# Optimization experiments

Hardware: AMD Instinct MI355X
Metric: run time of the kernel (lower is better)

The kernel has to match this reference:

```python
import jax, jax.numpy as jnp
import numpy as np

N_NODES = 100000
N_EDGES = 1600000
NODE_F = 8   # augmented node features
EDGE_F = 2   # augmented edge features
GLOB_F = 1
HID = 16
L = 3        # message passing steps

EDGE_IN = GLOB_F + EDGE_F + 2 * NODE_F   # 19
NODE_IN = GLOB_F + EDGE_F + NODE_F       # 11
GLOB_IN = EDGE_F + NODE_F + GLOB_F       # 11


def setup_inputs() -> dict:
    key = jax.random.key(0)
    ks = jax.random.split(key, 20)
    inp = {
        "x": jax.random.normal(ks[0], (N_NODES, NODE_F), dtype=jnp.float32),
        "edge_index": jax.random.randint(ks[1], (2, N_EDGES), 0, N_NODES, dtype=jnp.int32),
        "edge_attr": jax.random.normal(ks[2], (N_EDGES, EDGE_F), dtype=jnp.float32),
        "g": jax.random.normal(ks[3], (1, GLOB_F), dtype=jnp.float32),
    }
    s = 0.1
    inp["edge_W1"] = jax.random.normal(ks[4], (L, EDGE_IN, HID), dtype=jnp.float32) * s
    inp["edge_b1"] = jnp.zeros((L, HID), dtype=jnp.float32)
    inp["edge_W2"] = jax.random.normal(ks[5], (L, HID, EDGE_F), dtype=jnp.float32) * s
    inp["edge_b2"] = jnp.zeros((L, EDGE_F), dtype=jnp.float32)
    inp["node_W1"] = jax.random.normal(ks[6], (L, NODE_IN, HID), dtype=jnp.float32) * s
    inp["node_b1"] = jnp.zeros((L, HID), dtype=jnp.float32)
    inp["node_W2"] = jax.random.normal(ks[7], (L, HID, NODE_F), dtype=jnp.float32) * s
    inp["node_b2"] = jnp.zeros((L, NODE_F), dtype=jnp.float32)
    inp["glob_W1"] = jax.random.normal(ks[8], (L, GLOB_IN, HID), dtype=jnp.float32) * s
    inp["glob_b1"] = jnp.zeros((L, HID), dtype=jnp.float32)
    inp["glob_W2"] = jax.random.normal(ks[9], (L, HID, GLOB_F), dtype=jnp.float32) * s
    inp["glob_b2"] = jnp.zeros((L, GLOB_F), dtype=jnp.float32)
    return inp


def _mlp(h, W1, b1, W2, b2):
    # two-layer MLP with ReLU after first layer only (activate_final=False, no layer_norm)
    return jnp.maximum(h @ W1 + b1, 0.0) @ W2 + b2


def reference(x, edge_index, edge_attr, g,
              edge_W1, edge_b1, edge_W2, edge_b2,
              node_W1, node_b1, node_W2, node_b2,
              glob_W1, glob_b1, glob_W2, glob_b2):
    row, col = edge_index[0], edge_index[1]
    n = x.shape[0]
    for l in range(L):
        g_e = jnp.broadcast_to(g, (row.shape[0], GLOB_F))
        # edge block: gather node features along edges, concat, MLP -> [E, EDGE_F]
        e_in = jnp.concatenate([g_e, x[row], x[col], edge_attr], axis=1)
        edge_emb = _mlp(e_in, edge_W1[l], edge_b1[l], edge_W2[l], edge_b2[l])
        # sum-aggregate edge embeddings to source nodes
        agg = jax.ops.segment_sum(edge_emb, row, num_segments=n)
        g_n = jnp.broadcast_to(g, (n, GLOB_F))
        node_emb = _mlp(jnp.concatenate([g_n, x, agg], axis=1),
                        node_W1[l], node_b1[l], node_W2[l], node_b2[l])
        # global block on mean-aggregated edge/node embeddings
        edge_gl = jnp.mean(edge_emb, axis=0, keepdims=True)
        node_gl = jnp.mean(node_emb, axis=0, keepdims=True)
        g = _mlp(jnp.concatenate([node_gl, edge_gl, g], axis=1),
                 glob_W1[l], glob_b1[l], glob_W2[l], glob_b2[l])
        x, edge_attr = node_emb, edge_emb
    return x  # final node embeddings [N, NODE_F]
```

## Files before the change

### kernel.cpp

```cpp
#include <hip/hip_runtime.h>

#define NN 100000
#define NE 1600000
#define CH 4096
#define NCHUNK ((NE + CH - 1) / CH)
#define NBUCK ((NN + 255) / 256)

__device__ __forceinline__ float wave_red(float v) {
#pragma unroll
    for (int off = 32; off > 0; off >>= 1) v += __shfl_down(v, off, 64);
    return v;
}

__global__ __launch_bounds__(256) void hist_kernel(
    const int* __restrict__ ei, int* __restrict__ hist)
{
    __shared__ int h[NBUCK];
    int t = threadIdx.x, c = blockIdx.x;
    for (int b = t; b < NBUCK; b += 256) h[b] = 0;
    __syncthreads();
    int base = c * CH;
    for (int i = t; i < CH; i += 256) {
        int e = base + i;
        if (e < NE) atomicAdd(&h[ei[e] >> 8], 1);
    }
    __syncthreads();
    for (int b = t; b < NBUCK; b += 256) hist[c * NBUCK + b] = h[b];
}

__global__ __launch_bounds__(512) void bscan_kernel(
    const int* __restrict__ hist, int* __restrict__ baseT, int* __restrict__ colTotal)
{
    __shared__ int buf[2][512];
    int b = blockIdx.x, t = threadIdx.x;
    int v = (t < NCHUNK) ? hist[t * NBUCK + b] : 0;
    buf[0][t] = v;
    __syncthreads();
    int src = 0;
    for (int d = 1; d < 512; d <<= 1) {
        int nv = buf[src][t] + ((t >= d) ? buf[src][t - d] : 0);
        buf[src ^ 1][t] = nv;
        src ^= 1;
        __syncthreads();
    }
    if (t < NCHUNK) baseT[b * NCHUNK + t] = buf[src][t] - v;
    if (t == NCHUNK - 1) colTotal[b] = buf[src][t];
}

__global__ __launch_bounds__(512) void boff_kernel(
    const int* __restrict__ colTotal, int* __restrict__ b_off)
{
    __shared__ int buf[2][512];
    int t = threadIdx.x;
    int v = (t < NBUCK) ? colTotal[t] : 0;
    buf[0][t] = v;
    __syncthreads();
    int src = 0;
    for (int d = 1; d < 512; d <<= 1) {
        int nv = buf[src][t] + ((t >= d) ? buf[src][t - d] : 0);
        buf[src ^ 1][t] = nv;
        src ^= 1;
        __syncthreads();
    }
    if (t < NBUCK) b_off[t] = buf[src][t] - v;
    if (t == NBUCK - 1) b_off[NBUCK] = buf[src][t];
}

__global__ __launch_bounds__(256) void fillb_kernel(
    const int* __restrict__ ei, const float* __restrict__ eattr,
    const int* __restrict__ baseT, const int* __restrict__ b_off,
    float4* __restrict__ rec)
{
    __shared__ int sslot[NBUCK];
    int t = threadIdx.x, c = blockIdx.x;
    for (int b = t; b < NBUCK; b += 256)
        sslot[b] = b_off[b] + baseT[b * NCHUNK + c];
    __syncthreads();
    int base = c * CH;
    for (int i = t; i < CH; i += 256) {
        int e = base + i;
        if (e < NE) {
            int row = ei[e];
            int slot = atomicAdd(&sslot[row >> 8], 1);
            float2 ea = reinterpret_cast<const float2*>(eattr)[e];
            float4 v;
            v.x = __int_as_float(row);
            v.y = __int_as_float(ei[NE + e]);
            v.z = ea.x; v.w = ea.y;
            rec[slot] = v;
        }
    }
}

template <bool WRITE_REC, bool NEED_SUM>
__global__ __launch_bounds__(1024, 4) void fused_kernel(
    float4* __restrict__ rec, const int* __restrict__ b_off,
    const float* __restrict__ gptr,
    const float* __restrict__ eW1, const float* __restrict__ eB1,
    const float* __restrict__ eW2, const float* __restrict__ eB2,
    const float* __restrict__ xin,
    const float* __restrict__ nW1, const float* __restrict__ nB1,
    const float* __restrict__ nW2, const float* __restrict__ nB2,
    float* __restrict__ xout, float* __restrict__ sums)
{
    __shared__ float sPrT[16 * 256];
    __shared__ float sagg[256][2];
    __shared__ float redE[16][2];
    __shared__ float redN[4][8];
    int tid = threadIdx.x;
    if (tid < 512) ((float*)sagg)[tid] = 0.f;

    int n0 = blockIdx.x * 256;
    bool own = (tid < 256) && (n0 + tid < NN);
    if (own) {
        const float4* xi = reinterpret_cast<const float4*>(xin + (size_t)(n0 + tid) * 8);
        float4 a0 = xi[0], a1 = xi[1];
        float xv[8] = {a0.x, a0.y, a0.z, a0.w, a1.x, a1.y, a1.z, a1.w};
        float pr[16];
#pragma unroll
        for (int q = 0; q < 16; q++) pr[q] = 0.f;
#pragma unroll
        for (int k = 0; k < 8; k++) {
            float v = xv[k];
#pragma unroll
            for (int q = 0; q < 16; q++) pr[q] += v * eW1[(1 + k) * 16 + q];
        }
#pragma unroll
        for (int q = 0; q < 16; q++) sPrT[q * 256 + tid] = pr[q];
    }
    __syncthreads();

    int e0 = b_off[blockIdx.x], e1 = b_off[blockIdx.x + 1];

    float gval = gptr[0];
    float gterm[16];
#pragma unroll
    for (int q = 0; q < 16; q++) gterm[q] = eB1[q] + gval * eW1[q];

    float t0 = 0.f, t1 = 0.f;
    for (int e = e0 + tid; e < e1; e += 1024) {
        float4 r = rec[e];
        int row = __float_as_int(r.x);
        int col = __float_as_int(r.y);
        float ea0 = r.z, ea1 = r.w;
        int li = row - n0;
        const float4* xc4 = reinterpret_cast<const float4*>(xin + (size_t)col * 8);
        float4 c0 = xc4[0], c1 = xc4[1];
        float xc[8] = {c0.x, c0.y, c0.z, c0.w, c1.x, c1.y, c1.z, c1.w};
        float h[16];
#pragma unroll
        for (int q = 0; q < 16; q++) h[q] = gterm[q] + sPrT[q * 256 + li];
#pragma unroll
        for (int k = 0; k < 8; k++) {
            float v = xc[k];
#pragma unroll
            for (int q = 0; q < 16; q++) h[q] += v * eW1[(9 + k) * 16 + q];
        }
#pragma unroll
        for (int q = 0; q < 16; q++) {
            h[q] += ea0 * eW1[17 * 16 + q];
            h[q] += ea1 * eW1[18 * 16 + q];
        }
        float s0 = eB2[0], s1 = eB2[1];
#pragma unroll
        for (int q = 0; q < 16; q++) {
            float rr = fmaxf(h[q], 0.f);
            s0 += rr * eW2[2 * q];
            s1 += rr * eW2[2 * q + 1];
        }
        if (WRITE_REC) {
            float4 w;
            w.x = r.x; w.y = r.y; w.z = s0; w.w = s1;
            rec[e] = w;
        }
        atomicAdd(&sagg[li][0], s0);
        atomicAdd(&sagg[li][1], s1);
        t0 += s0; t1 += s1;
    }

    if (NEED_SUM) {
        float r0 = wave_red(t0);
        float r1 = wave_red(t1);
        int wave = tid >> 6, lane = tid & 63;
        if (lane == 0) { redE[wave][0] = r0; redE[wave][1] = r1; }
    }
    __syncthreads();
    if (NEED_SUM && tid == 0) {
        float s0 = 0.f, s1 = 0.f;
#pragma unroll
        for (int w = 0; w < 16; w++) { s0 += redE[w][0]; s1 += redE[w][1]; }
        atomicAdd(&sums[0], s0);
        atomicAdd(&sums[1], s1);
    }

    float out[8];
#pragma unroll
    for (int m = 0; m < 8; m++) out[m] = 0.f;

    if (own) {
        int n = n0 + tid;
        float in[11];
        in[0] = gval;
        const float4* xi = reinterpret_cast<const float4*>(xin + (size_t)n * 8);
        float4 a0 = xi[0], a1 = xi[1];
        in[1] = a0.x; in[2] = a0.y; in[3] = a0.z; in[4] = a0.w;
        in[5] = a1.x; in[6] = a1.y; in[7] = a1.z; in[8] = a1.w;
        in[9] = sagg[tid][0]; in[10] = sagg[tid][1];

        float h[16];
#pragma unroll
        for (int q = 0; q < 16; q++) h[q] = nB1[q];
#pragma unroll
        for (int k = 0; k < 11; k++) {
            float v = in[k];
#pragma unroll
            for (int q = 0; q < 16; q++) h[q] += v * nW1[k * 16 + q];
        }
#pragma unroll
        for (int m = 0; m < 8; m++) out[m] = nB2[m];
#pragma unroll
        for (int q = 0; q < 16; q++) {
            float hq = fmaxf(h[q], 0.f);
#pragma unroll
            for (int m = 0; m < 8; m++) out[m] += hq * nW2[q * 8 + m];
        }
        float4* xo = reinterpret_cast<float4*>(xout + (size_t)n * 8);
        xo[0] = make_float4(out[0], out[1], out[2], out[3]);
        xo[1] = make_float4(out[4], out[5], out[6], out[7]);
    }
    if (NEED_SUM) {
        float r[8];
#pragma unroll
        for (int m = 0; m < 8; m++) r[m] = wave_red(out[m]);
        int wave = tid >> 6, lane = tid & 63;
        if (wave < 4 && lane == 0) {
#pragma unroll
            for (int m = 0; m < 8; m++) redN[wave][m] = r[m];
        }
        __syncthreads();
        if (tid == 0) {
#pragma unroll
            for (int m = 0; m < 8; m++) {
                float s = redN[0][m] + redN[1][m] + redN[2][m] + redN[3][m];
                atomicAdd(&sums[2 + m], s);
            }
        }
    }
}

__global__ void glob_kernel(const float* __restrict__ sums,
                            const float* __restrict__ gold,
                            const float* __restrict__ W1, const float* __restrict__ B1,
                            const float* __restrict__ W2, const float* __restrict__ B2,
                            float* __restrict__ gnew)
{
    if (threadIdx.x == 0 && blockIdx.x == 0) {
        float in[11];
#pragma unroll
        for (int j = 0; j < 8; j++) in[j] = sums[2 + j] * (1.0f / NN);
        in[8] = sums[0] * (1.0f / NE);
        in[9] = sums[1] * (1.0f / NE);
        in[10] = gold[0];
        float acc = B2[0];
#pragma unroll
        for (int j = 0; j < 16; j++) {
            float h = B1[j];
#pragma unroll
            for (int k = 0; k < 11; k++) h += in[k] * W1[k * 16 + j];
            acc += fmaxf(h, 0.f) * W2[j];
        }
        gnew[0] = acc;
    }
}

extern "C" void kernel_launch(void* const* d_in, const int* in_sizes, int n_in,
                              void* d_out, int out_size, void* d_ws, size_t ws_size,
                              hipStream_t stream) {
    const float* x     = (const float*)d_in[0];
    const int*   ei    = (const int*)d_in[1];
    const float* eattr = (const float*)d_in[2];
    const float* g     = (const float*)d_in[3];
    const float* eW1 = (const float*)d_in[4];
    const float* eB1 = (const float*)d_in[5];
    const float* eW2 = (const float*)d_in[6];
    const float* eB2 = (const float*)d_in[7];
    const float* nW1 = (const float*)d_in[8];
    const float* nB1 = (const float*)d_in[9];
    const float* nW2 = (const float*)d_in[10];
    const float* nB2 = (const float*)d_in[11];
    const float* gW1 = (const float*)d_in[12];
    const float* gB1 = (const float*)d_in[13];
    const float* gW2 = (const float*)d_in[14];
    const float* gB2 = (const float*)d_in[15];
    float* out = (float*)d_out;

    char* ws = (char*)d_ws;
    float*  xb0   = (float*)(ws);
    float*  xb1   = (float*)(ws + 3200000);
    int*    b_off = (int*)  (ws + 6400000);
    float*  sums  = (float*)(ws + 6401600);
    float*  g1    = (float*)(ws + 6401728);
    float*  g2    = g1 + 1;
    float4* rec   = (float4*)(ws + 6401792);
    int*    hist     = (int*)xb1;
    int*    baseT    = (int*)((char*)xb1 + 611584);
    int*    colTotal = (int*)((char*)xb1 + 1223168);

    dim3 blk(256);
    dim3 fblk(1024);
    dim3 cgrid(NCHUNK);
    dim3 bgrid(NBUCK);

    hipMemsetAsync(sums, 0, 128, stream);
    hist_kernel<<<cgrid, blk, 0, stream>>>(ei, hist);
    bscan_kernel<<<bgrid, 512, 0, stream>>>(hist, baseT, colTotal);
    boff_kernel<<<1, 512, 0, stream>>>(colTotal, b_off);
    fillb_kernel<<<cgrid, blk, 0, stream>>>(ei, eattr, baseT, b_off, rec);

    fused_kernel<true, true><<<bgrid, fblk, 0, stream>>>(
        rec, b_off, g,
        eW1, eB1, eW2, eB2,
        x, nW1, nB1, nW2, nB2,
        xb0, sums);
    glob_kernel<<<1, 64, 0, stream>>>(sums, g, gW1, gB1, gW2, gB2, g1);

    fused_kernel<true, true><<<bgrid, fblk, 0, stream>>>(
        rec, b_off, g1,
        eW1 + 304, eB1 + 16, eW2 + 32, eB2 + 2,
        xb0, nW1 + 176, nB1 + 16, nW2 + 128, nB2 + 8,
        xb1, sums + 16);
    glob_kernel<<<1, 64, 0, stream>>>(sums + 16, g1, gW1 + 176, gB1 + 16, gW2 + 16, gB2 + 1, g2);

    fused_kernel<false, false><<<bgrid, fblk, 0, stream>>>(
        rec, b_off, g2,
        eW1 + 608, eB1 + 32, eW2 + 64, eB2 + 4,
        xb1, nW1 + 352, nB1 + 32, nW2 + 256, nB2 + 16,
        out, sums);
}
```

Measured before the change: 331.7 us.

## Split edge records into packed keys and attrs, double-buffer them into LDS

Replaces the 16-byte per-edge record with a 4-byte packed key (local row plus column) and a separate float2 attribute/embedding array, which cuts per-edge read and write traffic. Edge chunks are staged into LDS with asynchronous global_load_lds and double-buffered so the next chunk loads while the current one computes. Block size drops from 1024 to 512, and the projected source-node features are stored row-major so each edge reads them as float4. The changes add per-chunk barriers. Layer 2 reads and writes eembS in place, which relies on each edge index being read and written by the same thread.

```diff
diff --git a/kernel.cpp b/kernel.cpp
--- a/kernel.cpp
+++ b/kernel.cpp
@@ -5,11 +5,19 @@
 #define CH 4096
 #define NCHUNK ((NE + CH - 1) / CH)
 #define NBUCK ((NN + 255) / 256)
+#define ECHUNK 1024
 
 __device__ __forceinline__ float wave_red(float v) {
 #pragma unroll
     for (int off = 32; off > 0; off >>= 1) v += __shfl_down(v, off, 64);
     return v;
+}
+
+__device__ __forceinline__ void stage16(void* lds, const void* gsrc) {
+    __builtin_amdgcn_global_load_lds(
+        (const __attribute__((address_space(1))) unsigned int*)gsrc,
+        (__attribute__((address_space(3))) unsigned int*)lds,
+        16, 0, 0);
 }
 
 __global__ __launch_bounds__(256) void hist_kernel(
@@ -69,7 +77,7 @@
 __global__ __launch_bounds__(256) void fillb_kernel(
     const int* __restrict__ ei, const float* __restrict__ eattr,
     const int* __restrict__ baseT, const int* __restrict__ b_off,
-    float4* __restrict__ rec)
+    int* __restrict__ keys, float2* __restrict__ attrS)
 {
     __shared__ int sslot[NBUCK];
     int t = threadIdx.x, c = blockIdx.x;
@@ -82,19 +90,17 @@
         if (e < NE) {
             int row = ei[e];
             int slot = atomicAdd(&sslot[row >> 8], 1);
-            float2 ea = reinterpret_cast<const float2*>(eattr)[e];
-            float4 v;
-            v.x = __int_as_float(row);
-            v.y = __int_as_float(ei[NE + e]);
-            v.z = ea.x; v.w = ea.y;
-            rec[slot] = v;
-        }
-    }
-}
-
-template <bool WRITE_REC, bool NEED_SUM>
-__global__ __launch_bounds__(1024, 4) void fused_kernel(
-    float4* __restrict__ rec, const int* __restrict__ b_off,
+            keys[slot] = ((row & 255) << 17) | ei[NE + e];
+            attrS[slot] = reinterpret_cast<const float2*>(eattr)[e];
+        }
+    }
+}
+
+template <bool WRITE_EMB, bool NEED_SUM>
+__global__ __launch_bounds__(512, 4) void fused_kernel(
+    const int* __restrict__ keys,
+    const float2* __restrict__ ein, float2* __restrict__ eout,
+    const int* __restrict__ b_off,
     const float* __restrict__ gptr,
     const float* __restrict__ eW1, const float* __restrict__ eB1,
     const float* __restrict__ eW2, const float* __restrict__ eB2,
@@ -103,19 +109,24 @@
     const float* __restrict__ nW2, const float* __restrict__ nB2,
     float* __restrict__ xout, float* __restrict__ sums)
 {
-    __shared__ float sPrT[16 * 256];
-    __shared__ float sagg[256][2];
-    __shared__ float redE[16][2];
-    __shared__ float redN[4][8];
+    __shared__ float  sPr[256][20];
+    __shared__ float  sagg[256][2];
+    __shared__ int    kbuf[2][ECHUNK];
+    __shared__ float2 abuf[2][ECHUNK];
+    __shared__ float  redE[8][2];
+    __shared__ float  redN[4][8];
     int tid = threadIdx.x;
-    if (tid < 512) ((float*)sagg)[tid] = 0.f;
+    ((float*)sagg)[tid] = 0.f;
 
     int n0 = blockIdx.x * 256;
+    float gval = gptr[0];
     bool own = (tid < 256) && (n0 + tid < NN);
+    float xv[8];
     if (own) {
         const float4* xi = reinterpret_cast<const float4*>(xin + (size_t)(n0 + tid) * 8);
         float4 a0 = xi[0], a1 = xi[1];
-        float xv[8] = {a0.x, a0.y, a0.z, a0.w, a1.x, a1.y, a1.z, a1.w};
+        xv[0] = a0.x; xv[1] = a0.y; xv[2] = a0.z; xv[3] = a0.w;
+        xv[4] = a1.x; xv[5] = a1.y; xv[6] = a1.z; xv[7] = a1.w;
         float pr[16];
 #pragma unroll
         for (int q = 0; q < 16; q++) pr[q] = 0.f;
@@ -125,62 +136,82 @@
 #pragma unroll
             for (int q = 0; q < 16; q++) pr[q] += v * eW1[(1 + k) * 16 + q];
         }
-#pragma unroll
-        for (int q = 0; q < 16; q++) sPrT[q * 256 + tid] = pr[q];
-    }
-    __syncthreads();
+        float4* pw = reinterpret_cast<float4*>(&sPr[tid][0]);
+#pragma unroll
+        for (int t4 = 0; t4 < 4; t4++)
+            pw[t4] = make_float4(pr[4*t4], pr[4*t4+1], pr[4*t4+2], pr[4*t4+3]);
+    }
 
     int e0 = b_off[blockIdx.x], e1 = b_off[blockIdx.x + 1];
-
-    float gval = gptr[0];
+    int a0 = e0 & ~3;
+    int nc = (e1 - a0 + ECHUNK - 1) / ECHUNK;
+
+    if (tid < 256) stage16(&kbuf[0][tid * 4], keys + a0 + tid * 4);
+    stage16(&abuf[0][tid * 2], ein + a0 + tid * 2);
+
     float gterm[16];
 #pragma unroll
     for (int q = 0; q < 16; q++) gterm[q] = eB1[q] + gval * eW1[q];
 
     float t0 = 0.f, t1 = 0.f;
-    for (int e = e0 + tid; e < e1; e += 1024) {
-        float4 r = rec[e];
-        int row = __float_as_int(r.x);
-        int col = __float_as_int(r.y);
-        float ea0 = r.z, ea1 = r.w;
-        int li = row - n0;
-        const float4* xc4 = reinterpret_cast<const float4*>(xin + (size_t)col * 8);
-        float4 c0 = xc4[0], c1 = xc4[1];
-        float xc[8] = {c0.x, c0.y, c0.z, c0.w, c1.x, c1.y, c1.z, c1.w};
-        float h[16];
-#pragma unroll
-        for (int q = 0; q < 16; q++) h[q] = gterm[q] + sPrT[q * 256 + li];
-#pragma unroll
-        for (int k = 0; k < 8; k++) {
-            float v = xc[k];
-#pragma unroll
-            for (int q = 0; q < 16; q++) h[q] += v * eW1[(9 + k) * 16 + q];
-        }
-#pragma unroll
-        for (int q = 0; q < 16; q++) {
-            h[q] += ea0 * eW1[17 * 16 + q];
-            h[q] += ea1 * eW1[18 * 16 + q];
-        }
-        float s0 = eB2[0], s1 = eB2[1];
-#pragma unroll
-        for (int q = 0; q < 16; q++) {
-            float rr = fmaxf(h[q], 0.f);
-            s0 += rr * eW2[2 * q];
-            s1 += rr * eW2[2 * q + 1];
-        }
-        if (WRITE_REC) {
-            float4 w;
-            w.x = r.x; w.y = r.y; w.z = s0; w.w = s1;
-            rec[e] = w;
-        }
-        atomicAdd(&sagg[li][0], s0);
-        atomicAdd(&sagg[li][1], s1);
-        t0 += s0; t1 += s1;
+    for (int c = 0; c < nc; c++) {
+        __syncthreads();
+        int cur = c & 1;
+        if (c + 1 < nc) {
+            int wb = a0 + (c + 1) * ECHUNK;
+            if (tid < 256) stage16(&kbuf[cur ^ 1][tid * 4], keys + wb + tid * 4);
+            stage16(&abuf[cur ^ 1][tid * 2], ein + wb + tid * 2);
+        }
+        int cbase = a0 + c * ECHUNK;
+#pragma unroll
+        for (int j = 0; j < 2; j++) {
+            int idx = tid + j * 512;
+            int e = cbase + idx;
+            if (e < e0 || e >= e1) continue;
+            int k = kbuf[cur][idx];
+            float2 ea = abuf[cur][idx];
+            int li = k >> 17, col = k & 0x1FFFF;
+            const float4* xc4 = reinterpret_cast<const float4*>(xin + (size_t)col * 8);
+            float4 c0 = xc4[0], c1 = xc4[1];
+            const float4* pr4 = reinterpret_cast<const float4*>(&sPr[li][0]);
+            float4 p0 = pr4[0], p1 = pr4[1], p2 = pr4[2], p3 = pr4[3];
+            float h[16];
+            h[0]  = gterm[0]  + p0.x; h[1]  = gterm[1]  + p0.y;
+            h[2]  = gterm[2]  + p0.z; h[3]  = gterm[3]  + p0.w;
+            h[4]  = gterm[4]  + p1.x; h[5]  = gterm[5]  + p1.y;
+            h[6]  = gterm[6]  + p1.z; h[7]  = gterm[7]  + p1.w;
+            h[8]  = gterm[8]  + p2.x; h[9]  = gterm[9]  + p2.y;
+            h[10] = gterm[10] + p2.z; h[11] = gterm[11] + p2.w;
+            h[12] = gterm[12] + p3.x; h[13] = gterm[13] + p3.y;
+            h[14] = gterm[14] + p3.z; h[15] = gterm[15] + p3.w;
+            float xc[8] = {c0.x, c0.y, c0.z, c0.w, c1.x, c1.y, c1.z, c1.w};
+#pragma unroll
+            for (int kk = 0; kk < 8; kk++) {
+                float v = xc[kk];
+#pragma unroll
+                for (int q = 0; q < 16; q++) h[q] += v * eW1[(9 + kk) * 16 + q];
+            }
+#pragma unroll
+            for (int q = 0; q < 16; q++) {
+                h[q] += ea.x * eW1[17 * 16 + q];
+                h[q] += ea.y * eW1[18 * 16 + q];
+            }
+            float s0 = eB2[0], s1 = eB2[1];
+#pragma unroll
+            for (int q = 0; q < 16; q++) {
+                float rr = fmaxf(h[q], 0.f);
+                s0 += rr * eW2[2 * q];
+                s1 += rr * eW2[2 * q + 1];
+            }
+            if (WRITE_EMB) eout[e] = make_float2(s0, s1);
+            atomicAdd(&sagg[li][0], s0);
+            atomicAdd(&sagg[li][1], s1);
+            t0 += s0; t1 += s1;
+        }
     }
 
     if (NEED_SUM) {
-        float r0 = wave_red(t0);
-        float r1 = wave_red(t1);
+        float r0 = wave_red(t0), r1 = wave_red(t1);
         int wave = tid >> 6, lane = tid & 63;
         if (lane == 0) { redE[wave][0] = r0; redE[wave][1] = r1; }
     }
@@ -188,7 +219,7 @@
     if (NEED_SUM && tid == 0) {
         float s0 = 0.f, s1 = 0.f;
 #pragma unroll
-        for (int w = 0; w < 16; w++) { s0 += redE[w][0]; s1 += redE[w][1]; }
+        for (int w = 0; w < 8; w++) { s0 += redE[w][0]; s1 += redE[w][1]; }
         atomicAdd(&sums[0], s0);
         atomicAdd(&sums[1], s1);
     }
@@ -201,10 +232,8 @@
         int n = n0 + tid;
         float in[11];
         in[0] = gval;
-        const float4* xi = reinterpret_cast<const float4*>(xin + (size_t)n * 8);
-        float4 a0 = xi[0], a1 = xi[1];
-        in[1] = a0.x; in[2] = a0.y; in[3] = a0.z; in[4] = a0.w;
-        in[5] = a1.x; in[6] = a1.y; in[7] = a1.z; in[8] = a1.w;
+#pragma unroll
+        for (int k = 0; k < 8; k++) in[1 + k] = xv[k];
         in[9] = sagg[tid][0]; in[10] = sagg[tid][1];
 
         float h[16];
@@ -301,13 +330,15 @@
     float*  sums  = (float*)(ws + 6401600);
     float*  g1    = (float*)(ws + 6401728);
     float*  g2    = g1 + 1;
-    float4* rec   = (float4*)(ws + 6401792);
+    int*    keys  = (int*)  (ws + 6401792);
+    float2* attrS = (float2*)(ws + 12809984);
+    float2* eembS = (float2*)(ws + 25626368);
     int*    hist     = (int*)xb1;
     int*    baseT    = (int*)((char*)xb1 + 611584);
     int*    colTotal = (int*)((char*)xb1 + 1223168);
 
     dim3 blk(256);
-    dim3 fblk(1024);
+    dim3 fblk(512);
     dim3 cgrid(NCHUNK);
     dim3 bgrid(NBUCK);
 
@@ -315,24 +346,24 @@
     hist_kernel<<<cgrid, blk, 0, stream>>>(ei, hist);
     bscan_kernel<<<bgrid, 512, 0, stream>>>(hist, baseT, colTotal);
     boff_kernel<<<1, 512, 0, stream>>>(colTotal, b_off);
-    fillb_kernel<<<cgrid, blk, 0, stream>>>(ei, eattr, baseT, b_off, rec);
+    fillb_kernel<<<cgrid, blk, 0, stream>>>(ei, eattr, baseT, b_off, keys, attrS);
 
     fused_kernel<true, true><<<bgrid, fblk, 0, stream>>>(
-        rec, b_off, g,
+        keys, attrS, eembS, b_off, g,
         eW1, eB1, eW2, eB2,
         x, nW1, nB1, nW2, nB2,
         xb0, sums);
     glob_kernel<<<1, 64, 0, stream>>>(sums, g, gW1, gB1, gW2, gB2, g1);
 
     fused_kernel<true, true><<<bgrid, fblk, 0, stream>>>(
-        rec, b_off, g1,
+        keys, eembS, eembS, b_off, g1,
         eW1 + 304, eB1 + 16, eW2 + 32, eB2 + 2,
         xb0, nW1 + 176, nB1 + 16, nW2 + 128, nB2 + 8,
         xb1, sums + 16);
     glob_kernel<<<1, 64, 0, stream>>>(sums + 16, g1, gW1 + 176, gB1 + 16, gW2 + 16, gB2 + 1, g2);
 
     fused_kernel<false, false><<<bgrid, fblk, 0, stream>>>(
-        rec, b_off, g2,
+        keys, eembS, nullptr, b_off, g2,
         eW1 + 608, eB1 + 32, eW2 + 64, eB2 + 4,
         xb1, nW1 + 352, nB1 + 32, nW2 + 256, nB2 + 16,
         out, sums);
```

Result: slower. 343.3 us (+3.5%).
